# Kernel optimization log

Measured on AMD Instinct MI355X. Metric: run time of the kernel, lower is better.

The kernel has to match this reference:

```python
import jax, jax.numpy as jnp
import numpy as np

D_MODEL = 512
N_HEADS = 8
D_HEAD = D_MODEL // N_HEADS  # 64
D_PROJ = 32
H_ENC = 512
D_MAX = 32


def _rope_cache(T, d):
    pos = jnp.arange(T, dtype=jnp.float32)[:, None]                      # [T,1]
    freqs = 1.0 / (10000.0 ** (jnp.arange(0, d, 2, dtype=jnp.float32) / d))  # [d/2]
    ang = pos * freqs                                                     # [T,d/2]
    return jnp.cos(ang), jnp.sin(ang)


def _apply_rope(x, cos, sin):
    # x: [B,H,T,D]
    T = x.shape[2]
    d2 = x.shape[-1] // 2
    x1, x2 = x[..., :d2], x[..., d2:]
    c = cos[:T][None, None]
    s = sin[:T][None, None]
    return jnp.concatenate([x1 * c - x2 * s, x2 * c + x1 * s], axis=-1)


def _layernorm(a, g, b, eps=1e-5):
    m = jnp.mean(a, axis=-1, keepdims=True)
    v = jnp.mean((a - m) ** 2, axis=-1, keepdims=True)
    return (a - m) * jax.lax.rsqrt(v + eps) * g + b


def setup_inputs() -> dict:
    key = jax.random.key(0)
    ks = jax.random.split(key, 8)
    B, T = 2, 2048
    x = jax.random.normal(ks[0], (B, T, D_MODEL), jnp.float32)
    q_projs = jax.random.normal(ks[1], (N_HEADS, D_MODEL, D_PROJ), jnp.float32) * D_MODEL ** -0.5
    k_projs = jax.random.normal(ks[2], (N_HEADS, D_MODEL, D_PROJ), jnp.float32) * D_MODEL ** -0.5
    w_v = jax.random.normal(ks[3], (D_MODEL, D_MODEL), jnp.float32) * D_MODEL ** -0.5
    w_proj = jax.random.normal(ks[4], (D_MODEL, D_MODEL), jnp.float32) * 0.02
    q_gain = jnp.ones((N_HEADS,), jnp.float32)
    enc_w0 = jax.random.normal(ks[5], (H_ENC, D_MODEL), jnp.float32) * D_MODEL ** -0.5
    enc_ln1_g = jnp.ones((H_ENC,), jnp.float32)
    enc_ln1_b = jnp.zeros((H_ENC,), jnp.float32)
    enc_w1 = jax.random.normal(ks[6], (H_ENC, H_ENC), jnp.float32) * H_ENC ** -0.5
    enc_ln2_g = jnp.ones((H_ENC,), jnp.float32)
    enc_ln2_b = jnp.zeros((H_ENC,), jnp.float32)
    enc_w2 = jax.random.normal(ks[7], (H_ENC, H_ENC), jnp.float32) * H_ENC ** -0.5
    enc_w_out = jax.random.normal(jax.random.fold_in(key, 99), (D_MAX, H_ENC), jnp.float32) * H_ENC ** -0.5
    coord_temp = jnp.ones((D_MAX,), jnp.float32)
    return {"x": x, "q_projs": q_projs, "k_projs": k_projs, "w_v": w_v, "w_proj": w_proj,
            "q_gain": q_gain, "enc_w0": enc_w0, "enc_ln1_g": enc_ln1_g, "enc_ln1_b": enc_ln1_b,
            "enc_w1": enc_w1, "enc_ln2_g": enc_ln2_g, "enc_ln2_b": enc_ln2_b, "enc_w2": enc_w2,
            "enc_w_out": enc_w_out, "coord_temp": coord_temp}


def reference(x, q_projs, k_projs, w_v, w_proj, q_gain,
              enc_w0, enc_ln1_g, enc_ln1_b, enc_w1, enc_ln2_g, enc_ln2_b,
              enc_w2, enc_w_out, coord_temp):
    B, T, C = x.shape
    # ---- CausalSelfAttention (qk_mode='per_head_proj') ----
    q = jnp.einsum('btd,hdo->bhto', x, q_projs)                    # [B,H,T,Dp]
    k = jnp.einsum('btd,hdo->bhto', x, k_projs)                    # [B,H,T,Dp]
    v = (x @ w_v.T).reshape(B, T, N_HEADS, D_HEAD).transpose(0, 2, 1, 3)  # [B,H,T,Dh]
    cos, sin = _rope_cache(T, D_PROJ)
    q = _apply_rope(q, cos, sin)
    k = _apply_rope(k, cos, sin)
    q = q * q_gain[None, :, None, None]
    scale = 1.0 / jnp.sqrt(jnp.asarray(D_PROJ, q.dtype))
    scores = jnp.einsum('bhto,bhso->bhts', q, k) * scale           # [B,H,T,T]
    causal = jnp.tril(jnp.ones((T, T), bool))
    scores = jnp.where(causal, scores, jnp.asarray(-1e30, scores.dtype))
    attn = jax.nn.softmax(scores, axis=-1)
    y = jnp.einsum('bhts,bhsd->bhtd', attn, v)                     # [B,H,T,Dh]
    # self-alignment subtraction (F.normalize eps = 1e-12)
    v_norm = v / jnp.maximum(jnp.linalg.norm(v, axis=-1, keepdims=True), 1e-12)
    self_align = jnp.sum(y * v_norm, axis=-1, keepdims=True) * v_norm
    y = y - self_align
    y = y.transpose(0, 2, 1, 3).reshape(B, T, C)
    h = x + y @ w_proj.T                                           # residual
    # ---- ChartEncoder (d_in == H so proj0 is Identity) ----
    he = h @ enc_w0.T
    he = h + jax.nn.silu(_layernorm(he, enc_ln1_g, enc_ln1_b) @ enc_w1.T)
    he = he + jax.nn.silu(_layernorm(he, enc_ln2_g, enc_ln2_b) @ enc_w2.T)
    h_rms = he * jax.lax.rsqrt(jnp.mean(he * he, axis=-1, keepdims=True) + 1e-6)
    z_raw = h_rms @ enc_w_out.T                                    # [B,T,d_max]
    z = jnp.tanh(z_raw / (jax.nn.softplus(coord_temp) + 1e-4))
    return z
```

## Files before the change

### kernel.cpp

```cpp
#include <hip/hip_runtime.h>
#include <math.h>

typedef unsigned short u16;
typedef __attribute__((ext_vector_type(8))) short short8;
typedef __attribute__((ext_vector_type(4))) float floatx4;

__device__ __forceinline__ float b2f(u16 u) { return __uint_as_float(((unsigned)u) << 16); }
__device__ __forceinline__ u16 f2b(float f) {
  unsigned u = __float_as_uint(f);
  return (u16)((u + 0x7fffu + ((u >> 16) & 1u)) >> 16);
}

__global__ __launch_bounds__(256) void prep_cast(const float* __restrict__ x, const float* __restrict__ wpr,
                                                 const float* __restrict__ w0, const float* __restrict__ w1,
                                                 const float* __restrict__ w2, const float* __restrict__ qp,
                                                 const float* __restrict__ kp, const float* __restrict__ wv,
                                                 u16* __restrict__ XB, u16* __restrict__ WPRb,
                                                 u16* __restrict__ W0b, u16* __restrict__ W1b,
                                                 u16* __restrict__ W2b, u16* __restrict__ wcat) {
  int bi = blockIdx.x, tid = threadIdx.x;
  if (bi < 2048) {
    int i = bi * 256 + tid;
    float4 v = ((const float4*)x)[i];
    ushort4 o; o.x = f2b(v.x); o.y = f2b(v.y); o.z = f2b(v.z); o.w = f2b(v.w);
    ((ushort4*)XB)[i] = o;
  } else if (bi < 3072) {
    int i = (bi - 2048) * 256 + tid;
    int sel = i >> 16, j = i & 65535;
    const float* s = sel == 0 ? wpr : sel == 1 ? w0 : sel == 2 ? w1 : w2;
    float4 v = ((const float4*)s)[j];
    ushort4 o; o.x = f2b(v.x); o.y = f2b(v.y); o.z = f2b(v.z); o.w = f2b(v.w);
    if (sel == 0) {
      ((ushort4*)WPRb)[j] = o;
    } else {
      u16* d = sel == 1 ? W0b : sel == 2 ? W1b : W2b;
      int n = j >> 7, k4 = (j & 127) << 2;
      int lane = (((k4 >> 3) & 3) << 4) | (n & 15);
      int dst = (((n >> 4) * 16 + (k4 >> 5)) << 9) + lane * 8 + (k4 & 7);
      *(ushort4*)(d + dst) = o;
    }
  } else {
    int i = (bi - 3072) * 256 + tid;
    int d = i & 511, c = i >> 9;
    float v;
    if (c < 512) {
      int hh = c >> 5, o = c & 31;
      const float* src = (hh < 8) ? qp : kp;
      int h = hh & 7;
      v = src[(h * 512 + d) * 32 + o];
    } else {
      v = wv[(c - 512) * 512 + d];
    }
    wcat[i] = f2b(v);
  }
}

template <int EPI, bool DUAL>
__global__ __launch_bounds__(256) void mgemm(const u16* __restrict__ A, const u16* __restrict__ Bw,
                                             const float* __restrict__ X, float* __restrict__ C,
                                             u16* __restrict__ Cb, int N) {
  __shared__ u16 As[64][72];
  __shared__ u16 Bs[64][72];
  const int tid = threadIdx.x;
  const int bm = blockIdx.y, bn = blockIdx.x;
  const int lane = tid & 63, wave = tid >> 6;
  const int wm = wave >> 1, wn = wave & 1;
  const int quad = lane >> 4, l16 = lane & 15;
  const int sr = tid >> 2;
  const int sk = (tid & 3) << 4;
  floatx4 acc[2][2] = {};
  const u16* Ap = A + (size_t)(bm * 64 + sr) * 512 + sk;
  const u16* Bp = Bw + (size_t)(bn * 64 + sr) * 512 + sk;
  uint4 a0 = *(const uint4*)(Ap);
  uint4 a1 = *(const uint4*)(Ap + 8);
  uint4 b0 = *(const uint4*)(Bp);
  uint4 b1 = *(const uint4*)(Bp + 8);
  for (int k0 = 0; k0 < 512; k0 += 64) {
    __syncthreads();
    *(uint4*)&As[sr][sk] = a0;
    *(uint4*)&As[sr][sk + 8] = a1;
    *(uint4*)&Bs[sr][sk] = b0;
    *(uint4*)&Bs[sr][sk + 8] = b1;
    __syncthreads();
    if (k0 + 64 < 512) {
      a0 = *(const uint4*)(Ap + k0 + 64);
      a1 = *(const uint4*)(Ap + k0 + 72);
      b0 = *(const uint4*)(Bp + k0 + 64);
      b1 = *(const uint4*)(Bp + k0 + 72);
    }
#pragma unroll
    for (int kk = 0; kk < 2; kk++) {
      short8 af0 = *(const short8*)&As[wm * 32 + l16][kk * 32 + quad * 8];
      short8 af1 = *(const short8*)&As[wm * 32 + 16 + l16][kk * 32 + quad * 8];
      short8 bf0 = *(const short8*)&Bs[wn * 32 + l16][kk * 32 + quad * 8];
      short8 bf1 = *(const short8*)&Bs[wn * 32 + 16 + l16][kk * 32 + quad * 8];
      acc[0][0] = __builtin_amdgcn_mfma_f32_16x16x32_bf16(af0, bf0, acc[0][0], 0, 0, 0);
      acc[0][1] = __builtin_amdgcn_mfma_f32_16x16x32_bf16(af0, bf1, acc[0][1], 0, 0, 0);
      acc[1][0] = __builtin_amdgcn_mfma_f32_16x16x32_bf16(af1, bf0, acc[1][0], 0, 0, 0);
      acc[1][1] = __builtin_amdgcn_mfma_f32_16x16x32_bf16(af1, bf1, acc[1][1], 0, 0, 0);
    }
  }
#pragma unroll
  for (int mt = 0; mt < 2; mt++)
#pragma unroll
    for (int r = 0; r < 4; r++) {
      int row = bm * 64 + wm * 32 + mt * 16 + quad * 4 + r;
#pragma unroll
      for (int nt = 0; nt < 2; nt++) {
        int col = bn * 64 + wn * 32 + nt * 16 + l16;
        float v = acc[mt][nt][r];
        if (EPI == 1) {
          v += X[(size_t)row * 512 + col];
        } else if (EPI == 2) {
          float xv = X[(size_t)row * 512 + col];
          v = xv + v / (1.f + __expf(-v));
        }
        C[(size_t)row * N + col] = v;
        if (DUAL) Cb[(size_t)row * N + col] = f2b(v);
      }
    }
}

__global__ __launch_bounds__(256) void prep_attn(const float* __restrict__ qkv, const float* __restrict__ qgain,
                                                 u16* __restrict__ qr, u16* __restrict__ kr,
                                                 u16* __restrict__ Vt) {
  const int bi = blockIdx.x, tid = threadIdx.x;
  if (bi < 2048) {
    int gid = bi * 256 + tid;
    int o = gid & 15;
    int t = (gid >> 4) & 2047;
    int h = (gid >> 15) & 7;
    int b = gid >> 18;
    const float* row = qkv + (size_t)(b * 2048 + t) * 1024;
    float freq = powf(10000.f, -(float)o / 16.f);
    float ang = (float)t * freq;
    float s, c;
    sincosf(ang, &s, &c);
    float g = qgain[h] * (0.17677669529663687f * 1.4426950408889634f);
    int qb = h * 32;
    float q0 = row[qb + o], q1 = row[qb + o + 16];
    float k0 = row[256 + qb + o], k1 = row[256 + qb + o + 16];
    u16* qo = qr + ((size_t)((b * 8 + h) * 2048 + t)) * 32;
    u16* ko = kr + ((size_t)((b * 8 + h) * 2048 + t)) * 32;
    qo[o] = f2b((q0 * c - q1 * s) * g);
    qo[o + 16] = f2b((q1 * c + q0 * s) * g);
    ko[o] = f2b(k0 * c - k1 * s);
    ko[o + 16] = f2b(k1 * c + k0 * s);
  } else {
    int idx = bi - 2048;
    const int tt = idx & 31, bh = idx >> 5;
    const int b = bh >> 3, h = bh & 7;
    __shared__ u16 Ts[64][72];
    const int r = tid >> 2, q = tid & 3;
    const float* src = qkv + ((size_t)(b * 2048 + tt * 64 + r)) * 1024 + 512 + h * 64 + q * 16;
#pragma unroll
    for (int j = 0; j < 4; j++) {
      float4 v = *(const float4*)(src + j * 4);
      Ts[q * 16 + j * 4 + 0][r] = f2b(v.x);
      Ts[q * 16 + j * 4 + 1][r] = f2b(v.y);
      Ts[q * 16 + j * 4 + 2][r] = f2b(v.z);
      Ts[q * 16 + j * 4 + 3][r] = f2b(v.w);
    }
    __syncthreads();
    u16* dst = Vt + ((size_t)(bh * 64 + r)) * 2048 + tt * 64 + q * 16;
    *(uint4*)dst = *(const uint4*)&Ts[r][q * 16];
    *(uint4*)(dst + 8) = *(const uint4*)&Ts[r][q * 16 + 8];
  }
}

__global__ __launch_bounds__(256) void attn_split(const u16* __restrict__ Qb, const u16* __restrict__ Kb,
                                                  const u16* __restrict__ Vt, float* __restrict__ PO,
                                                  float* __restrict__ PL) {
  const int bi = blockIdx.x;
  const int bh = bi & 15;
  const int q0i = (bi >> 4) & 15;
  const int rem = bi >> 8;
  const int qt = (rem & 1) ? (31 - q0i) : q0i;
  const int s = rem >> 1;
  const int tid = threadIdx.x;
  const int w = tid >> 6, lane = tid & 63, quad = lane >> 4, l16 = lane & 15;
  __shared__ u16 Vts[64][72];
  __shared__ u16 Ps[4][16][72];

  const int mid = (qt + 1) >> 1;
  const int kt_beg = s ? mid : 0;
  const int kt_end = s ? (qt + 1) : mid;

  short8 qfrag = *(const short8*)(Qb + ((size_t)(bh * 2048 + qt * 64 + w * 16 + l16)) * 32 + quad * 8);
  floatx4 o_acc[4] = {};
  float l_part[4] = {0.f, 0.f, 0.f, 0.f};
  const u16* Kbase = Kb + (size_t)bh * 2048 * 32;
  const u16* Vtb = Vt + (size_t)bh * 64 * 2048;
  const int vr = tid >> 2, vc = (tid & 3) << 4;

  uint4 v0 = {}, v1 = {};
  short8 kf[4] = {};
  if (kt_beg < kt_end) {
    const u16* src = Vtb + (size_t)vr * 2048 + kt_beg * 64 + vc;
    v0 = *(const uint4*)src;
    v1 = *(const uint4*)(src + 8);
#pragma unroll
    for (int nt = 0; nt < 4; nt++)
      kf[nt] = *(const short8*)(Kbase + (size_t)(kt_beg * 64 + nt * 16 + l16) * 32 + quad * 8);
  }

  for (int kt = kt_beg; kt < kt_end; ++kt) {
    __syncthreads();
    *(uint4*)&Vts[vr][vc] = v0;
    *(uint4*)&Vts[vr][vc + 8] = v1;
    __syncthreads();
    const bool more = (kt + 1 < kt_end);
    uint4 v0n = {}, v1n = {};
    short8 kfn[4] = {};
    if (more) {
      const u16* src = Vtb + (size_t)vr * 2048 + (kt + 1) * 64 + vc;
      v0n = *(const uint4*)src;
      v1n = *(const uint4*)(src + 8);
#pragma unroll
      for (int nt = 0; nt < 4; nt++)
        kfn[nt] = *(const short8*)(Kbase + (size_t)((kt + 1) * 64 + nt * 16 + l16) * 32 + quad * 8);
    }

    floatx4 s_acc[4];
    __builtin_amdgcn_s_setprio(1);
#pragma unroll
    for (int nt = 0; nt < 4; nt++) {
      floatx4 zz = {0.f, 0.f, 0.f, 0.f};
      s_acc[nt] = __builtin_amdgcn_mfma_f32_16x16x32_bf16(qfrag, kf[nt], zz, 0, 0, 0);
    }
    __builtin_amdgcn_s_setprio(0);
    const bool diag = (kt == qt);
#pragma unroll
    for (int r = 0; r < 4; r++) {
      int mloc = w * 16 + quad * 4 + r;
      float psum = 0.f;
#pragma unroll
      for (int nt = 0; nt < 4; nt++) {
        float p = __builtin_amdgcn_exp2f(s_acc[nt][r]);
        if (diag && (nt * 16 + l16) > mloc) p = 0.f;
        psum += p;
        Ps[w][quad * 4 + r][nt * 16 + l16] = f2b(p);
      }
      l_part[r] += psum;
    }
    __builtin_amdgcn_s_setprio(1);
#pragma unroll
    for (int kc = 0; kc < 2; kc++) {
      short8 pf = *(const short8*)&Ps[w][l16][kc * 32 + quad * 8];
#pragma unroll
      for (int nt = 0; nt < 4; nt++) {
        short8 vf = *(const short8*)&Vts[nt * 16 + l16][kc * 32 + quad * 8];
        o_acc[nt] = __builtin_amdgcn_mfma_f32_16x16x32_bf16(pf, vf, o_acc[nt], 0, 0, 0);
      }
    }
    __builtin_amdgcn_s_setprio(0);
    v0 = v0n; v1 = v1n;
#pragma unroll
    for (int nt = 0; nt < 4; nt++) kf[nt] = kfn[nt];
  }

  const int pidx = (bh * 32 + qt) * 2 + s;
  float* pob = PO + (size_t)pidx * 4096;
#pragma unroll
  for (int r = 0; r < 4; r++) {
    float ls = l_part[r];
#pragma unroll
    for (int mk = 1; mk < 16; mk <<= 1) ls += __shfl_xor(ls, mk, 64);
    int row = w * 16 + quad * 4 + r;
#pragma unroll
    for (int nt = 0; nt < 4; nt++) pob[row * 64 + nt * 16 + l16] = o_acc[nt][r];
    if (l16 == 0) PL[pidx * 64 + row] = ls;
  }
}

__global__ __launch_bounds__(256) void attn_combine(const float* __restrict__ PO, const float* __restrict__ PL,
                                                    const float* __restrict__ qkv, u16* __restrict__ y2b) {
  int ridx = blockIdx.x * 4 + (threadIdx.x >> 6);
  int lane = threadIdx.x & 63;
  int bh = ridx >> 11, tok = ridx & 2047;
  int qt = tok >> 6, row = tok & 63;
  int pidx = (bh * 32 + qt) * 2;
  const float* p0 = PO + (size_t)pidx * 4096 + row * 64;
  float o = p0[lane] + p0[4096 + lane];
  float l = PL[pidx * 64 + row] + PL[(pidx + 1) * 64 + row];
  float yv = o / l;
  int b = bh >> 3, h = bh & 7;
  float vv = qkv[(size_t)(b * 2048 + tok) * 1024 + 512 + h * 64 + lane];
  float ss = vv * vv, dot = yv * vv;
#pragma unroll
  for (int mk = 1; mk < 64; mk <<= 1) {
    ss += __shfl_xor(ss, mk, 64);
    dot += __shfl_xor(dot, mk, 64);
  }
  float coef = dot / fmaxf(ss, 1e-24f);
  y2b[(size_t)(b * 2048 + tok) * 512 + h * 64 + lane] = f2b(yv - coef * vv);
}

#define HPAD 516

__device__ __forceinline__ int enc_swz(int row, int col) {
  return row * 512 + ((((col >> 3) ^ (row & 7)) << 3) | (col & 7));
}

__device__ __forceinline__ void enc_gemm(const u16* __restrict__ inb, const u16* __restrict__ Wf,
                                         floatx4* acc, int wave, int l16, int quad, int lane, int krot) {
  const u16* wb = Wf + ((size_t)(wave * 4 * 16) << 9) + lane * 8;
  short8 aB[4];
  short8 bB[4][4];
#pragma unroll
  for (int p = 0; p < 4; p++) {
    const int kc = (p + krot) & 15;
    aB[p] = *(const short8*)(inb + enc_swz(l16, kc * 32 + quad * 8));
#pragma unroll
    for (int nt = 0; nt < 4; nt++)
      bB[p][nt] = *(const short8*)(wb + (((nt * 16) + kc) << 9));
  }
#pragma unroll
  for (int ks = 0; ks < 16; ks++) {
    const int cur = ks & 3;
#pragma unroll
    for (int nt = 0; nt < 4; nt++)
      acc[nt] = __builtin_amdgcn_mfma_f32_16x16x32_bf16(aB[cur], bB[cur][nt], acc[nt], 0, 0, 0);
    if (ks + 4 < 16) {
      const int kn = (ks + 4 + krot) & 15;
      aB[cur] = *(const short8*)(inb + enc_swz(l16, kn * 32 + quad * 8));
#pragma unroll
      for (int nt = 0; nt < 4; nt++)
        bB[cur][nt] = *(const short8*)(wb + (((nt * 16) + kn) << 9));
    }
  }
}

__global__ __launch_bounds__(512) void enc_fused(const float* __restrict__ H, const u16* __restrict__ W0b,
                                                 const u16* __restrict__ W1b, const u16* __restrict__ W2b,
                                                 const float* __restrict__ g1v, const float* __restrict__ b1v,
                                                 const float* __restrict__ g2v, const float* __restrict__ b2v,
                                                 const float* __restrict__ wout, const float* __restrict__ ct,
                                                 float* __restrict__ z) {
  __shared__ u16 curb[16 * 512];
  __shared__ u16 lnb[16 * 512];
  __shared__ float hres[16][HPAD];
  __shared__ float red[8][16][2];

  const int tid = threadIdx.x;
  const int wave = tid >> 6, lane = tid & 63, quad = lane >> 4, l16 = lane & 15;
  const int row0 = blockIdx.x * 16;
  const int n0 = wave * 64;
  const int krot = (blockIdx.x >> 3) & 15;

#pragma unroll
  for (int j = 0; j < 4; j++) {
    int idx = j * 512 + tid;
    int row = idx >> 7, c4 = idx & 127;
    float4 v = ((const float4*)H)[(size_t)(row0 + row) * 128 + c4];
    *(float4*)&hres[row][c4 * 4] = v;
    int col = c4 * 4;
    curb[enc_swz(row, col + 0)] = f2b(v.x);
    curb[enc_swz(row, col + 1)] = f2b(v.y);
    curb[enc_swz(row, col + 2)] = f2b(v.z);
    curb[enc_swz(row, col + 3)] = f2b(v.w);
  }
  __syncthreads();

  floatx4 acc1[4] = {};
  enc_gemm(curb, W0b, acc1, wave, l16, quad, lane, krot);

  {
#pragma unroll
    for (int r = 0; r < 4; r++) {
      float s = 0.f, q = 0.f;
#pragma unroll
      for (int nt = 0; nt < 4; nt++) { float v = acc1[nt][r]; s += v; q = fmaf(v, v, q); }
#pragma unroll
      for (int mk = 1; mk < 16; mk <<= 1) { s += __shfl_xor(s, mk, 64); q += __shfl_xor(q, mk, 64); }
      if (l16 == 0) { red[wave][quad * 4 + r][0] = s; red[wave][quad * 4 + r][1] = q; }
    }
    __syncthreads();
#pragma unroll
    for (int r = 0; r < 4; r++) {
      int R = quad * 4 + r;
      float st = 0.f, qt2 = 0.f;
#pragma unroll
      for (int w2 = 0; w2 < 8; w2++) { st += red[w2][R][0]; qt2 += red[w2][R][1]; }
      float mean = st * (1.f / 512.f);
      float inv = rsqrtf(qt2 * (1.f / 512.f) - mean * mean + 1e-5f);
#pragma unroll
      for (int nt = 0; nt < 4; nt++) {
        int col = n0 + nt * 16 + l16;
        lnb[enc_swz(R, col)] = f2b((acc1[nt][r] - mean) * inv * g1v[col] + b1v[col]);
      }
    }
    __syncthreads();
  }

  floatx4 acc2[4] = {};
  enc_gemm(lnb, W1b, acc2, wave, l16, quad, lane, krot);
  float hval[4][4];
  {
#pragma unroll
    for (int r = 0; r < 4; r++) {
      int R = quad * 4 + r;
      float s = 0.f, q = 0.f;
#pragma unroll
      for (int nt = 0; nt < 4; nt++) {
        int col = n0 + nt * 16 + l16;
        float u = acc2[nt][r];
        float hv = hres[R][col] + u / (1.f + __expf(-u));
        hres[R][col] = hv;
        hval[nt][r] = hv;
        s += hv; q = fmaf(hv, hv, q);
      }
#pragma unroll
      for (int mk = 1; mk < 16; mk <<= 1) { s += __shfl_xor(s, mk, 64); q += __shfl_xor(q, mk, 64); }
      if (l16 == 0) { red[wave][R][0] = s; red[wave][R][1] = q; }
    }
    __syncthreads();
#pragma unroll
    for (int r = 0; r < 4; r++) {
      int R = quad * 4 + r;
      float st = 0.f, qt2 = 0.f;
#pragma unroll
      for (int w2 = 0; w2 < 8; w2++) { st += red[w2][R][0]; qt2 += red[w2][R][1]; }
      float mean = st * (1.f / 512.f);
      float inv = rsqrtf(qt2 * (1.f / 512.f) - mean * mean + 1e-5f);
#pragma unroll
      for (int nt = 0; nt < 4; nt++) {
        int col = n0 + nt * 16 + l16;
        lnb[enc_swz(R, col)] = f2b((hval[nt][r] - mean) * inv * g2v[col] + b2v[col]);
      }
    }
    __syncthreads();
  }

  floatx4 acc3[4] = {};
  enc_gemm(lnb, W2b, acc3, wave, l16, quad, lane, krot);
  {
#pragma unroll
    for (int r = 0; r < 4; r++) {
      int R = quad * 4 + r;
      float q = 0.f;
#pragma unroll
      for (int nt = 0; nt < 4; nt++) {
        int col = n0 + nt * 16 + l16;
        float u = acc3[nt][r];
        float hv = hres[R][col] + u / (1.f + __expf(-u));
        hres[R][col] = hv;
        q = fmaf(hv, hv, q);
      }
#pragma unroll
      for (int mk = 1; mk < 16; mk <<= 1) q += __shfl_xor(q, mk, 64);
      if (l16 == 0) red[wave][R][1] = q;
    }
    __syncthreads();
  }

  {
    const int n = lane & 31, kh = lane >> 5;
    float rinv[2], pacc[2] = {0.f, 0.f};
#pragma unroll
    for (int rr = 0; rr < 2; rr++) {
      int R = wave * 2 + rr;
      float qt2 = 0.f;
#pragma unroll
      for (int w2 = 0; w2 < 8; w2++) qt2 += red[w2][R][1];
      rinv[rr] = rsqrtf(qt2 * (1.f / 512.f) + 1e-6f);
    }
    for (int kc = 0; kc < 64; kc++) {
      int k = kh * 256 + kc * 4;
      float4 wv = *(const float4*)(wout + (size_t)n * 512 + k);
#pragma unroll
      for (int rr = 0; rr < 2; rr++) {
        float4 hv = *(const float4*)&hres[wave * 2 + rr][k];
        pacc[rr] = fmaf(wv.x, hv.x, fmaf(wv.y, hv.y, fmaf(wv.z, hv.z, fmaf(wv.w, hv.w, pacc[rr]))));
      }
    }
#pragma unroll
    for (int rr = 0; rr < 2; rr++) pacc[rr] += __shfl_xor(pacc[rr], 32, 64);
    if (kh == 0) {
      float c = ct[n];
      float sp = (c > 20.f) ? c : log1pf(__expf(c));
#pragma unroll
      for (int rr = 0; rr < 2; rr++)
        z[(size_t)(row0 + wave * 2 + rr) * 32 + n] = tanhf(pacc[rr] * rinv[rr] / (sp + 1e-4f));
    }
  }
}

extern "C" void kernel_launch(void* const* d_in, const int* in_sizes, int n_in,
                              void* d_out, int out_size, void* d_ws, size_t ws_size,
                              hipStream_t stream) {
  const float* x = (const float*)d_in[0];
  const float* qp = (const float*)d_in[1];
  const float* kp = (const float*)d_in[2];
  const float* wv = (const float*)d_in[3];
  const float* wpr = (const float*)d_in[4];
  const float* qg = (const float*)d_in[5];
  const float* w0 = (const float*)d_in[6];
  const float* g1 = (const float*)d_in[7];
  const float* b1 = (const float*)d_in[8];
  const float* w1 = (const float*)d_in[9];
  const float* g2 = (const float*)d_in[10];
  const float* b2 = (const float*)d_in[11];
  const float* w2 = (const float*)d_in[12];
  const float* wout = (const float*)d_in[13];
  const float* ct = (const float*)d_in[14];
  float* z = (float*)d_out;

  float* ws = (float*)d_ws;
  const size_t MEG = 1024 * 1024;
  float* A_QKV = ws;
  u16* A_Qb = (u16*)(ws + 4 * MEG);
  u16* A_Kb = (u16*)(ws + 4 * MEG + 524288);
  u16* A_Vt = (u16*)(ws + 5 * MEG);
  float* A_PO = ws + 6 * MEG;
  u16* A_Y2b = (u16*)(ws + 10 * MEG);
  float* A_H = ws + 11 * MEG;
  u16* XB = (u16*)(ws + 13 * MEG);
  float* A_PL = ws + 13 * MEG;
  u16* WCATb = (u16*)(ws + 14 * MEG);
  u16* WPRb = WCATb + 524288;
  u16* W0b = WPRb + 262144;
  u16* W1b = W0b + 262144;
  u16* W2b = W1b + 262144;

  hipLaunchKernelGGL(prep_cast, dim3(5120), dim3(256), 0, stream, x, wpr, w0, w1, w2, qp, kp, wv,
                     XB, WPRb, W0b, W1b, W2b, WCATb);
  hipLaunchKernelGGL((mgemm<0, false>), dim3(16, 64), dim3(256), 0, stream, XB, WCATb,
                     (const float*)nullptr, A_QKV, (u16*)nullptr, 1024);
  hipLaunchKernelGGL(prep_attn, dim3(2560), dim3(256), 0, stream, A_QKV, qg, A_Qb, A_Kb, A_Vt);
  hipLaunchKernelGGL(attn_split, dim3(1024), dim3(256), 0, stream, A_Qb, A_Kb, A_Vt, A_PO, A_PL);
  hipLaunchKernelGGL(attn_combine, dim3(8192), dim3(256), 0, stream, A_PO, A_PL, A_QKV, A_Y2b);
  hipLaunchKernelGGL((mgemm<1, false>), dim3(8, 64), dim3(256), 0, stream, A_Y2b, WPRb, x, A_H,
                     (u16*)nullptr, 512);
  hipLaunchKernelGGL(enc_fused, dim3(256), dim3(512), 0, stream, A_H, W0b, W1b, W2b,
                     g1, b1, g2, b2, wout, ct, z);
}
```

Measured before the change: 185.2 us.

## Fuse RoPE, Q scaling and V transpose into the QKV GEMM epilogue

The separate prep_attn kernel is removed and its work moves into a dedicated QKV GEMM epilogue. Q/K tiles get RoPE (and Q gain scaling) applied directly from accumulators and are written as bf16. V tiles are written both as fp32 for the self-alignment step and transposed to bf16 through shared memory. This drops one launch and the fp32 QKV round trip, at the cost of per-element sincos in the GEMM epilogue and scattered 2-byte stores.

```diff
diff --git a/kernel.cpp b/kernel.cpp
--- a/kernel.cpp
+++ b/kernel.cpp
@@ -121,50 +121,108 @@
     }
 }
 
-__global__ __launch_bounds__(256) void prep_attn(const float* __restrict__ qkv, const float* __restrict__ qgain,
-                                                 u16* __restrict__ qr, u16* __restrict__ kr,
-                                                 u16* __restrict__ Vt) {
-  const int bi = blockIdx.x, tid = threadIdx.x;
-  if (bi < 2048) {
-    int gid = bi * 256 + tid;
-    int o = gid & 15;
-    int t = (gid >> 4) & 2047;
-    int h = (gid >> 15) & 7;
-    int b = gid >> 18;
-    const float* row = qkv + (size_t)(b * 2048 + t) * 1024;
-    float freq = powf(10000.f, -(float)o / 16.f);
-    float ang = (float)t * freq;
-    float s, c;
-    sincosf(ang, &s, &c);
-    float g = qgain[h] * (0.17677669529663687f * 1.4426950408889634f);
-    int qb = h * 32;
-    float q0 = row[qb + o], q1 = row[qb + o + 16];
-    float k0 = row[256 + qb + o], k1 = row[256 + qb + o + 16];
-    u16* qo = qr + ((size_t)((b * 8 + h) * 2048 + t)) * 32;
-    u16* ko = kr + ((size_t)((b * 8 + h) * 2048 + t)) * 32;
-    qo[o] = f2b((q0 * c - q1 * s) * g);
-    qo[o + 16] = f2b((q1 * c + q0 * s) * g);
-    ko[o] = f2b(k0 * c - k1 * s);
-    ko[o + 16] = f2b(k1 * c + k0 * s);
+__global__ __launch_bounds__(256) void qkv_gemm(const u16* __restrict__ A, const u16* __restrict__ Bw,
+                                                const float* __restrict__ qgain,
+                                                u16* __restrict__ Qb, u16* __restrict__ Kb,
+                                                u16* __restrict__ Vt, float* __restrict__ Vf) {
+  __shared__ u16 As[64][72];
+  __shared__ u16 Bs[64][72];
+  const int tid = threadIdx.x;
+  const int bm = blockIdx.y, bn = blockIdx.x;
+  const int lane = tid & 63, wave = tid >> 6;
+  const int wm = wave >> 1, wn = wave & 1;
+  const int quad = lane >> 4, l16 = lane & 15;
+  const int sr = tid >> 2;
+  const int sk = (tid & 3) << 4;
+  floatx4 acc[2][2] = {};
+  const u16* Ap = A + (size_t)(bm * 64 + sr) * 512 + sk;
+  const u16* Bp = Bw + (size_t)(bn * 64 + sr) * 512 + sk;
+  uint4 a0 = *(const uint4*)(Ap);
+  uint4 a1 = *(const uint4*)(Ap + 8);
+  uint4 b0 = *(const uint4*)(Bp);
+  uint4 b1 = *(const uint4*)(Bp + 8);
+  for (int k0 = 0; k0 < 512; k0 += 64) {
+    __syncthreads();
+    *(uint4*)&As[sr][sk] = a0;
+    *(uint4*)&As[sr][sk + 8] = a1;
+    *(uint4*)&Bs[sr][sk] = b0;
+    *(uint4*)&Bs[sr][sk + 8] = b1;
+    __syncthreads();
+    if (k0 + 64 < 512) {
+      a0 = *(const uint4*)(Ap + k0 + 64);
+      a1 = *(const uint4*)(Ap + k0 + 72);
+      b0 = *(const uint4*)(Bp + k0 + 64);
+      b1 = *(const uint4*)(Bp + k0 + 72);
+    }
+#pragma unroll
+    for (int kk = 0; kk < 2; kk++) {
+      short8 af0 = *(const short8*)&As[wm * 32 + l16][kk * 32 + quad * 8];
+      short8 af1 = *(const short8*)&As[wm * 32 + 16 + l16][kk * 32 + quad * 8];
+      short8 bf0 = *(const short8*)&Bs[wn * 32 + l16][kk * 32 + quad * 8];
+      short8 bf1 = *(const short8*)&Bs[wn * 32 + 16 + l16][kk * 32 + quad * 8];
+      acc[0][0] = __builtin_amdgcn_mfma_f32_16x16x32_bf16(af0, bf0, acc[0][0], 0, 0, 0);
+      acc[0][1] = __builtin_amdgcn_mfma_f32_16x16x32_bf16(af0, bf1, acc[0][1], 0, 0, 0);
+      acc[1][0] = __builtin_amdgcn_mfma_f32_16x16x32_bf16(af1, bf0, acc[1][0], 0, 0, 0);
+      acc[1][1] = __builtin_amdgcn_mfma_f32_16x16x32_bf16(af1, bf1, acc[1][1], 0, 0, 0);
+    }
+  }
+  if (bn < 8) {
+    const bool isq = (bn < 4);
+    const int h = (isq ? bn : bn - 4) * 2 + wn;
+    const float gq = isq ? qgain[h] * (0.17677669529663687f * 1.4426950408889634f) : 1.f;
+    const float freq = powf(10000.f, -(float)l16 / 16.f);
+    u16* outb = (isq ? Qb : Kb);
+#pragma unroll
+    for (int mt = 0; mt < 2; mt++)
+#pragma unroll
+      for (int r = 0; r < 4; r++) {
+        int row = bm * 64 + wm * 32 + mt * 16 + quad * 4 + r;
+        int t = row & 2047, b = row >> 11;
+        float s, c;
+        sincosf((float)t * freq, &s, &c);
+        float q0 = acc[mt][0][r], q1 = acc[mt][1][r];
+        u16* base = outb + ((size_t)((b * 8 + h) * 2048 + t)) * 32;
+        if (isq) {
+          base[l16] = f2b((q0 * c - q1 * s) * gq);
+          base[l16 + 16] = f2b((q1 * c + q0 * s) * gq);
+        } else {
+          base[l16] = f2b(q0 * c - q1 * s);
+          base[l16 + 16] = f2b(q1 * c + q0 * s);
+        }
+      }
   } else {
-    int idx = bi - 2048;
-    const int tt = idx & 31, bh = idx >> 5;
-    const int b = bh >> 3, h = bh & 7;
-    __shared__ u16 Ts[64][72];
-    const int r = tid >> 2, q = tid & 3;
-    const float* src = qkv + ((size_t)(b * 2048 + tt * 64 + r)) * 1024 + 512 + h * 64 + q * 16;
-#pragma unroll
-    for (int j = 0; j < 4; j++) {
-      float4 v = *(const float4*)(src + j * 4);
-      Ts[q * 16 + j * 4 + 0][r] = f2b(v.x);
-      Ts[q * 16 + j * 4 + 1][r] = f2b(v.y);
-      Ts[q * 16 + j * 4 + 2][r] = f2b(v.z);
-      Ts[q * 16 + j * 4 + 3][r] = f2b(v.w);
-    }
-    __syncthreads();
-    u16* dst = Vt + ((size_t)(bh * 64 + r)) * 2048 + tt * 64 + q * 16;
-    *(uint4*)dst = *(const uint4*)&Ts[r][q * 16];
-    *(uint4*)(dst + 8) = *(const uint4*)&Ts[r][q * 16 + 8];
+    const int h = bn - 8;
+    const int b = bm >> 5;
+#pragma unroll
+    for (int mt = 0; mt < 2; mt++)
+#pragma unroll
+      for (int r = 0; r < 4; r++) {
+        int row = bm * 64 + wm * 32 + mt * 16 + quad * 4 + r;
+#pragma unroll
+        for (int nt = 0; nt < 2; nt++) {
+          int d = wn * 32 + nt * 16 + l16;
+          Vf[(size_t)row * 512 + h * 64 + d] = acc[mt][nt][r];
+        }
+      }
+    __syncthreads();
+#pragma unroll
+    for (int mt = 0; mt < 2; mt++)
+#pragma unroll
+      for (int r = 0; r < 4; r++) {
+        int rl = wm * 32 + mt * 16 + quad * 4 + r;
+#pragma unroll
+        for (int nt = 0; nt < 2; nt++) {
+          int d = wn * 32 + nt * 16 + l16;
+          As[d][rl] = f2b(acc[mt][nt][r]);
+        }
+      }
+    __syncthreads();
+    const int bh = b * 8 + h;
+    const int t0 = (bm & 31) * 64;
+    const int dim = tid >> 2, ch = (tid & 3) << 4;
+    u16* dst = Vt + ((size_t)(bh * 64 + dim)) * 2048 + t0 + ch;
+    *(uint4*)dst = *(const uint4*)&As[dim][ch];
+    *(uint4*)(dst + 8) = *(const uint4*)&As[dim][ch + 8];
   }
 }
 
@@ -274,7 +332,7 @@
 }
 
 __global__ __launch_bounds__(256) void attn_combine(const float* __restrict__ PO, const float* __restrict__ PL,
-                                                    const float* __restrict__ qkv, u16* __restrict__ y2b) {
+                                                    const float* __restrict__ Vf, u16* __restrict__ y2b) {
   int ridx = blockIdx.x * 4 + (threadIdx.x >> 6);
   int lane = threadIdx.x & 63;
   int bh = ridx >> 11, tok = ridx & 2047;
@@ -285,7 +343,7 @@
   float l = PL[pidx * 64 + row] + PL[(pidx + 1) * 64 + row];
   float yv = o / l;
   int b = bh >> 3, h = bh & 7;
-  float vv = qkv[(size_t)(b * 2048 + tok) * 1024 + 512 + h * 64 + lane];
+  float vv = Vf[(size_t)(b * 2048 + tok) * 512 + h * 64 + lane];
   float ss = vv * vv, dot = yv * vv;
 #pragma unroll
   for (int mk = 1; mk < 64; mk <<= 1) {
@@ -508,7 +566,7 @@
 
   float* ws = (float*)d_ws;
   const size_t MEG = 1024 * 1024;
-  float* A_QKV = ws;
+  float* A_V = ws;
   u16* A_Qb = (u16*)(ws + 4 * MEG);
   u16* A_Kb = (u16*)(ws + 4 * MEG + 524288);
   u16* A_Vt = (u16*)(ws + 5 * MEG);
@@ -525,11 +583,10 @@
 
   hipLaunchKernelGGL(prep_cast, dim3(5120), dim3(256), 0, stream, x, wpr, w0, w1, w2, qp, kp, wv,
                      XB, WPRb, W0b, W1b, W2b, WCATb);
-  hipLaunchKernelGGL((mgemm<0, false>), dim3(16, 64), dim3(256), 0, stream, XB, WCATb,
-                     (const float*)nullptr, A_QKV, (u16*)nullptr, 1024);
-  hipLaunchKernelGGL(prep_attn, dim3(2560), dim3(256), 0, stream, A_QKV, qg, A_Qb, A_Kb, A_Vt);
+  hipLaunchKernelGGL(qkv_gemm, dim3(16, 64), dim3(256), 0, stream, XB, WCATb, qg,
+                     A_Qb, A_Kb, A_Vt, A_V);
   hipLaunchKernelGGL(attn_split, dim3(1024), dim3(256), 0, stream, A_Qb, A_Kb, A_Vt, A_PO, A_PL);
-  hipLaunchKernelGGL(attn_combine, dim3(8192), dim3(256), 0, stream, A_PO, A_PL, A_QKV, A_Y2b);
+  hipLaunchKernelGGL(attn_combine, dim3(8192), dim3(256), 0, stream, A_PO, A_PL, A_V, A_Y2b);
   hipLaunchKernelGGL((mgemm<1, false>), dim3(8, 64), dim3(256), 0, stream, A_Y2b, WPRb, x, A_H,
                      (u16*)nullptr, 512);
   hipLaunchKernelGGL(enc_fused, dim3(256), dim3(512), 0, stream, A_H, W0b, W1b, W2b,
```

Result: faster. 181.0 us (-2.3%).
